# Optimization experiments

Measured on AMD Instinct MI355X. Metric: run time of the kernel, lower is better.

## Reference

```python
import jax, jax.numpy as jnp
import numpy as np

N_NODES = 50000
N_EDGES = 800000
IN, HID, OUT = 128, 128, 64


def gcn_layer(x, W, b, src, dst, n):
    """PyG GCNConv: add self-loops, symmetric normalization, linear, scatter-add, bias."""
    loop = jnp.arange(n, dtype=src.dtype)
    s = jnp.concatenate([src, loop])  # message sources
    d = jnp.concatenate([dst, loop])  # message destinations
    deg = jax.ops.segment_sum(jnp.ones(s.shape[0], dtype=x.dtype), d, num_segments=n)
    dinv = jnp.where(deg > 0, jax.lax.rsqrt(deg), jnp.zeros_like(deg))
    norm = dinv[s] * dinv[d]  # [E+N]
    h = x @ W                 # dense transform first (PyG order)
    agg = jax.ops.segment_sum(h[s] * norm[:, None], d, num_segments=n)  # [N, out]
    return agg + b


def setup_inputs() -> dict:
    key = jax.random.key(0)
    ks = jax.random.split(key, 8)
    x = jax.random.normal(ks[0], (N_NODES, IN), dtype=jnp.float32)
    edge_index = jax.random.randint(ks[1], (2, N_EDGES), 0, N_NODES, dtype=jnp.int32)
    s = 0.05
    W1 = jax.random.normal(ks[2], (IN, HID), dtype=jnp.float32) * s
    b1 = jnp.zeros((HID,), dtype=jnp.float32)
    W2 = jax.random.normal(ks[3], (HID, HID), dtype=jnp.float32) * s
    b2 = jnp.zeros((HID,), dtype=jnp.float32)
    W3 = jax.random.normal(ks[4], (HID, OUT), dtype=jnp.float32) * s
    b3 = jnp.zeros((OUT,), dtype=jnp.float32)
    return {"x": x, "edge_index": edge_index, "W1": W1, "b1": b1,
            "W2": W2, "b2": b2, "W3": W3, "b3": b3}


def reference(x, edge_index, W1, b1, W2, b2, W3, b3):
    src, dst = edge_index[0], edge_index[1]
    n = x.shape[0]
    # dropout is identity in eval mode; ReLU follows every layer (incl. last) as in source
    h = jax.nn.relu(gcn_layer(x, W1, b1, src, dst, n))
    h = jax.nn.relu(gcn_layer(h, W2, b2, src, dst, n))
    h = jax.nn.relu(gcn_layer(h, W3, b3, src, dst, n))
    return jax.nn.log_softmax(h, axis=1)
```

## Files before the change

### kernel.cpp

```cpp
#include <hip/hip_runtime.h>
#include <math.h>


typedef __attribute__((ext_vector_type(8))) short short8;
typedef __attribute__((ext_vector_type(4))) float f32x4;

#define PADROW 50115
#define CAP 64
#define NPART 8

__device__ inline unsigned short f2bf(float x) {
    unsigned int u = __float_as_uint(x);
    u += 0x7fffu + ((u >> 16) & 1u);
    return (unsigned short)(u >> 16);
}
__device__ inline float blo(unsigned int v) { return __uint_as_float(v << 16); }
__device__ inline float bhi(unsigned int v) { return __uint_as_float(v & 0xffff0000u); }


__global__ void prep0_kernel(int* __restrict__ deg, int N,
                             unsigned int* __restrict__ col32, int colw,
                             const float* __restrict__ W1, unsigned short* __restrict__ W1t,
                             const float* __restrict__ W2, unsigned short* __restrict__ W2t,
                             const float* __restrict__ W3, unsigned short* __restrict__ W3t,
                             unsigned short* __restrict__ hbuf) {
    int i = blockIdx.x * blockDim.x + threadIdx.x;
    if (i < N) deg[i] = 0;
    if (i < colw) col32[i] = 0xC3C3C3C3u;
    if (i < 16384) {
        int k = i >> 7, n = i & 127;
        W1t[(size_t)n * 128 + k] = f2bf(W1[i]);
    } else if (i < 32768) {
        int j = i - 16384;
        int k = j >> 7, n = j & 127;
        W2t[(size_t)n * 128 + k] = f2bf(W2[j]);
    } else if (i < 40960) {
        int j = i - 32768;
        int k = j >> 6, n = j & 63;
        W3t[(size_t)n * 128 + k] = f2bf(W3[j]);
    }
    if (i < 16)
        ((uint4*)(hbuf + (size_t)PADROW * 128))[i] = make_uint4(0, 0, 0, 0);
}

__global__ void hist_rank_kernel(const int* __restrict__ dst, int* __restrict__ deg,
                                 unsigned short* __restrict__ rank, int E) {
    int e = blockIdx.x * blockDim.x + threadIdx.x;
    if (e < E) rank[e] = (unsigned short)atomicAdd(&deg[dst[e]], 1);
}

__global__ void scatter_ell_kernel(const int* __restrict__ src, const int* __restrict__ dst,
                                   const unsigned short* __restrict__ rank,
                                   unsigned short* __restrict__ col_ell,
                                   int E, int N, int nblk_per_part) {
    int part = blockIdx.x & (NPART - 1);
    int blk  = blockIdx.x / NPART;
    int npr = (N + NPART - 1) / NPART;
    int lo = part * npr;
    int hi = min(N, lo + npr);
    int stride = nblk_per_part * blockDim.x;
    for (int e = blk * blockDim.x + threadIdx.x; e < E; e += stride) {
        int d = dst[e];
        if (d >= lo && d < hi) {
            int rk = (int)rank[e];
            if (rk < CAP) col_ell[(size_t)d * CAP + rk] = (unsigned short)src[e];
        }
    }
}

template<int H, bool AF32>
__global__ __launch_bounds__(256) void gemm_mfma(const void* __restrict__ Av,
                                                 const unsigned short* __restrict__ Wt,
                                                 const int* __restrict__ deg,
                                                 unsigned short* __restrict__ C, int M) {
    __shared__ __attribute__((aligned(16))) unsigned short As[128][136];
    __shared__ __attribute__((aligned(16))) unsigned short Ws[H][136];
    int tid = threadIdx.x;
    int row0 = blockIdx.x * 128;
    if (AF32) {
        const float* A = (const float*)Av;
        #pragma unroll
        for (int g = tid; g < 128 * 32; g += 256) {
            int r = g >> 5, c = g & 31;
            int gr = row0 + r;
            ushort4 o = make_ushort4(0, 0, 0, 0);
            if (gr < M) {
                float4 v = *(const float4*)(A + (size_t)gr * 128 + c * 4);
                o.x = f2bf(v.x); o.y = f2bf(v.y); o.z = f2bf(v.z); o.w = f2bf(v.w);
            }
            *(ushort4*)&As[r][c * 4] = o;
        }
    } else {
        const unsigned short* A = (const unsigned short*)Av;
        #pragma unroll
        for (int g = tid; g < 128 * 16; g += 256) {
            int r = g >> 4, c = g & 15;
            int gr = row0 + r;
            uint4 v = make_uint4(0, 0, 0, 0);
            if (gr < M) v = *(const uint4*)(A + (size_t)gr * 128 + c * 8);
            *(uint4*)&As[r][c * 8] = v;
        }
    }
    #pragma unroll
    for (int g = tid; g < H * 16; g += 256) {
        int r = g >> 4, c = g & 15;
        *(uint4*)&Ws[r][c * 8] = *(const uint4*)(Wt + (size_t)r * 128 + c * 8);
    }
    if (H == 64 && blockIdx.x == 0 && tid < 8)
        ((uint4*)(C + (size_t)PADROW * 64))[tid] = make_uint4(0, 0, 0, 0);
    __syncthreads();

    int wave = tid >> 6, lane = tid & 63;
    int lr = lane & 15;
    int lk = (lane >> 4) * 8;

    short8 af[2][4];
    float dv[2][4];
    #pragma unroll
    for (int t = 0; t < 2; ++t) {
        int base = wave * 32 + t * 16;
        #pragma unroll
        for (int ks = 0; ks < 4; ++ks)
            af[t][ks] = *(const short8*)&As[base + lr][ks * 32 + lk];
        #pragma unroll
        for (int r = 0; r < 4; ++r) {
            int grow = row0 + base + (lane >> 4) * 4 + r;
            dv[t][r] = (grow < M) ? rsqrtf((float)deg[grow] + 1.0f) : 0.0f;
        }
    }

    #pragma unroll
    for (int ct = 0; ct < H / 16; ++ct) {
        f32x4 acc0 = {0.f, 0.f, 0.f, 0.f};
        f32x4 acc1 = {0.f, 0.f, 0.f, 0.f};
        #pragma unroll
        for (int ks = 0; ks < 4; ++ks) {
            short8 wf = *(const short8*)&Ws[ct * 16 + lr][ks * 32 + lk];
            acc0 = __builtin_amdgcn_mfma_f32_16x16x32_bf16(af[0][ks], wf, acc0, 0, 0, 0);
            acc1 = __builtin_amdgcn_mfma_f32_16x16x32_bf16(af[1][ks], wf, acc1, 0, 0, 0);
        }
        int gcol = ct * 16 + lr;
        #pragma unroll
        for (int r = 0; r < 4; ++r) {
            int g0 = row0 + wave * 32 + (lane >> 4) * 4 + r;
            if (g0 < M) C[(size_t)g0 * H + gcol] = f2bf(acc0[r] * dv[0][r]);
            int g1 = g0 + 16;
            if (g1 < M) C[(size_t)g1 * H + gcol] = f2bf(acc1[r] * dv[1][r]);
        }
    }
}

__global__ __launch_bounds__(256) void spmm128_kernel(const uint2* __restrict__ h2,
                                                      const unsigned short* __restrict__ col_ell,
                                                      const int* __restrict__ deg,
                                                      const float* __restrict__ bias,
                                                      uint2* __restrict__ out2, int N) {
    int wid = blockIdx.x * 4 + (threadIdx.x >> 6);
    int lane = threadIdx.x & 63;
    if (wid >= N) return;
    int half = lane >> 5;
    int c    = lane & 31;
    size_t base = (size_t)wid * CAP;
    int dg = deg[wid];
    float a0 = 0.f, a1 = 0.f, a2 = 0.f, a3 = 0.f;
    if (half == 0) {
        uint2 hv = h2[(size_t)wid * 32 + c];
        a0 = blo(hv.x); a1 = bhi(hv.x); a2 = blo(hv.y); a3 = bhi(hv.y);
    }
    {
        int s[12]; uint2 g[12];
        #pragma unroll
        for (int u = 0; u < 12; ++u) s[u] = (int)col_ell[base + 2 * u + half];
        #pragma unroll
        for (int u = 0; u < 12; ++u) g[u] = h2[(size_t)s[u] * 32 + c];
        #pragma unroll
        for (int u = 0; u < 12; ++u) {
            a0 += blo(g[u].x); a1 += bhi(g[u].x);
            a2 += blo(g[u].y); a3 += bhi(g[u].y);
        }
    }
    if (dg > 24) {
        int s[12]; uint2 g[12];
        #pragma unroll
        for (int u = 0; u < 12; ++u) s[u] = (int)col_ell[base + 24 + 2 * u + half];
        #pragma unroll
        for (int u = 0; u < 12; ++u) g[u] = h2[(size_t)s[u] * 32 + c];
        #pragma unroll
        for (int u = 0; u < 12; ++u) {
            a0 += blo(g[u].x); a1 += bhi(g[u].x);
            a2 += blo(g[u].y); a3 += bhi(g[u].y);
        }
        if (dg > 48) {
            int s[8]; uint2 g[8];
            #pragma unroll
            for (int u = 0; u < 8; ++u) s[u] = (int)col_ell[base + 48 + 2 * u + half];
            #pragma unroll
            for (int u = 0; u < 8; ++u) g[u] = h2[(size_t)s[u] * 32 + c];
            #pragma unroll
            for (int u = 0; u < 8; ++u) {
                a0 += blo(g[u].x); a1 += bhi(g[u].x);
                a2 += blo(g[u].y); a3 += bhi(g[u].y);
            }
        }
    }
    a0 += __shfl_xor(a0, 32);
    a1 += __shfl_xor(a1, 32);
    a2 += __shfl_xor(a2, 32);
    a3 += __shfl_xor(a3, 32);
    float dv = rsqrtf((float)dg + 1.0f);
    float4 b4 = ((const float4*)bias)[c];
    a0 = fmaxf(fmaf(a0, dv, b4.x), 0.0f);
    a1 = fmaxf(fmaf(a1, dv, b4.y), 0.0f);
    a2 = fmaxf(fmaf(a2, dv, b4.z), 0.0f);
    a3 = fmaxf(fmaf(a3, dv, b4.w), 0.0f);
    if (half == 0) {
        uint2 o;
        o.x = (unsigned int)f2bf(a0) | ((unsigned int)f2bf(a1) << 16);
        o.y = (unsigned int)f2bf(a2) | ((unsigned int)f2bf(a3) << 16);
        out2[(size_t)wid * 32 + c] = o;
    }
}

__global__ __launch_bounds__(256) void spmm64_lsm_kernel(const unsigned int* __restrict__ h1,
                                                         const unsigned short* __restrict__ col_ell,
                                                         const int* __restrict__ deg,
                                                         const float* __restrict__ bias,
                                                         float2* __restrict__ out2, int N) {
    int wid = blockIdx.x * 4 + (threadIdx.x >> 6);
    int lane = threadIdx.x & 63;
    if (wid >= N) return;
    int half = lane >> 5;
    int c    = lane & 31;
    size_t base = (size_t)wid * CAP;
    int dg = deg[wid];
    float a0 = 0.f, a1 = 0.f;
    if (half == 0) {
        unsigned int hv = h1[(size_t)wid * 32 + c];
        a0 = blo(hv); a1 = bhi(hv);
    }
    {
        int s[12]; unsigned int g[12];
        #pragma unroll
        for (int u = 0; u < 12; ++u) s[u] = (int)col_ell[base + 2 * u + half];
        #pragma unroll
        for (int u = 0; u < 12; ++u) g[u] = h1[(size_t)s[u] * 32 + c];
        #pragma unroll
        for (int u = 0; u < 12; ++u) { a0 += blo(g[u]); a1 += bhi(g[u]); }
    }
    if (dg > 24) {
        int s[12]; unsigned int g[12];
        #pragma unroll
        for (int u = 0; u < 12; ++u) s[u] = (int)col_ell[base + 24 + 2 * u + half];
        #pragma unroll
        for (int u = 0; u < 12; ++u) g[u] = h1[(size_t)s[u] * 32 + c];
        #pragma unroll
        for (int u = 0; u < 12; ++u) { a0 += blo(g[u]); a1 += bhi(g[u]); }
        if (dg > 48) {
            int s[8]; unsigned int g[8];
            #pragma unroll
            for (int u = 0; u < 8; ++u) s[u] = (int)col_ell[base + 48 + 2 * u + half];
            #pragma unroll
            for (int u = 0; u < 8; ++u) g[u] = h1[(size_t)s[u] * 32 + c];
            #pragma unroll
            for (int u = 0; u < 8; ++u) { a0 += blo(g[u]); a1 += bhi(g[u]); }
        }
    }
    a0 += __shfl_xor(a0, 32);
    a1 += __shfl_xor(a1, 32);
    float dv = rsqrtf((float)dg + 1.0f);
    float2 b2 = ((const float2*)bias)[c];
    a0 = fmaxf(fmaf(a0, dv, b2.x), 0.0f);
    a1 = fmaxf(fmaf(a1, dv, b2.y), 0.0f);
    float m = fmaxf(a0, a1);
    #pragma unroll
    for (int off = 16; off; off >>= 1) m = fmaxf(m, __shfl_xor(m, off));
    float ssum = expf(a0 - m) + expf(a1 - m);
    #pragma unroll
    for (int off = 16; off; off >>= 1) ssum += __shfl_xor(ssum, off);
    float lse = m + logf(ssum);
    if (half == 0) {
        float2 o;
        o.x = a0 - lse;
        o.y = a1 - lse;
        out2[(size_t)wid * 32 + c] = o;
    }
}


extern "C" void kernel_launch(void* const* d_in, const int* in_sizes, int n_in,
                              void* d_out, int out_size, void* d_ws, size_t ws_size,
                              hipStream_t stream) {
    const float* x  = (const float*)d_in[0];
    const int*   ei = (const int*)d_in[1];
    const float* W1 = (const float*)d_in[2];
    const float* b1 = (const float*)d_in[3];
    const float* W2 = (const float*)d_in[4];
    const float* b2 = (const float*)d_in[5];
    const float* W3 = (const float*)d_in[6];
    const float* b3 = (const float*)d_in[7];
    float* out = (float*)d_out;

    const int IN = 128, HID = 128, OUT = 64;
    int N = in_sizes[0] / IN;
    int E = in_sizes[1] / 2;
    const int* srcp = ei;
    const int* dstp = ei + E;

    char* p = (char*)d_ws;
    auto alloc = [&](size_t bytes) {
        char* r = p;
        p += (bytes + 255) & ~(size_t)255;
        return r;
    };
    int* deg = (int*)alloc((size_t)N * 4);
    unsigned short* rank16  = (unsigned short*)alloc((size_t)E * 2);
    unsigned short* col_ell = (unsigned short*)alloc((size_t)N * CAP * 2);
    unsigned short* W1t  = (unsigned short*)alloc((size_t)IN * HID * 2);
    unsigned short* W2t  = (unsigned short*)alloc((size_t)HID * HID * 2);
    unsigned short* W3t  = (unsigned short*)alloc((size_t)HID * OUT * 2);
    unsigned short* hbuf = (unsigned short*)alloc((size_t)(PADROW + 1) * HID * 2);
    unsigned short* abuf = (unsigned short*)alloc((size_t)N * HID * 2);

    int colw = N * CAP / 2;
    int prep0_grid = (max(colw, 40960) + 255) / 256;
    prep0_kernel<<<prep0_grid, 256, 0, stream>>>(deg, N, (unsigned int*)col_ell, colw,
                                                 W1, W1t, W2, W2t, W3, W3t, hbuf);
    hist_rank_kernel<<<(E + 255) / 256, 256, 0, stream>>>(dstp, deg, rank16, E);
    int nblk_per_part = 512;
    scatter_ell_kernel<<<NPART * nblk_per_part, 256, 0, stream>>>(srcp, dstp, rank16,
                                                                  col_ell, E, N, nblk_per_part);

    int nwave_blocks = (N + 3) / 4;
    int gemm_blocks = (N + 127) / 128;

    gemm_mfma<128, true><<<gemm_blocks, 256, 0, stream>>>(x, W1t, deg, hbuf, N);
    spmm128_kernel<<<nwave_blocks, 256, 0, stream>>>((const uint2*)hbuf, col_ell, deg,
                                                     b1, (uint2*)abuf, N);
    gemm_mfma<128, false><<<gemm_blocks, 256, 0, stream>>>(abuf, W2t, deg, hbuf, N);
    spmm128_kernel<<<nwave_blocks, 256, 0, stream>>>((const uint2*)hbuf, col_ell, deg,
                                                     b2, (uint2*)abuf, N);
    gemm_mfma<64, false><<<gemm_blocks, 256, 0, stream>>>(abuf, W3t, deg, hbuf, N);
    spmm64_lsm_kernel<<<nwave_blocks, 256, 0, stream>>>((const unsigned int*)hbuf, col_ell, deg,
                                                        b3, (float2*)out, N);
}
```

Measured before the change: 181.8 us.

## Fuse ELL histogram into scatter and remap spmm64 to one node per half-wave

Merges the histogram/rank kernel into the partitioned ELL scatter kernel, so each edge takes its slot with an atomicAdd on deg directly. This drops one launch and the rank buffer's write and read. It also changes the final spmm64+log_softmax kernel so that each 32-lane half-wave handles one node, instead of a full wave split into two halves. Each half-wave now gathers all neighbors itself, which removes the cross-half shuffle. The cost is more registers from the 24-wide unroll and longer serial gather chains per node.

```diff
diff --git a/kernel.cpp b/kernel.cpp
--- a/kernel.cpp
+++ b/kernel.cpp
@@ -43,16 +43,9 @@
         ((uint4*)(hbuf + (size_t)PADROW * 128))[i] = make_uint4(0, 0, 0, 0);
 }
 
-__global__ void hist_rank_kernel(const int* __restrict__ dst, int* __restrict__ deg,
-                                 unsigned short* __restrict__ rank, int E) {
-    int e = blockIdx.x * blockDim.x + threadIdx.x;
-    if (e < E) rank[e] = (unsigned short)atomicAdd(&deg[dst[e]], 1);
-}
-
-__global__ void scatter_ell_kernel(const int* __restrict__ src, const int* __restrict__ dst,
-                                   const unsigned short* __restrict__ rank,
-                                   unsigned short* __restrict__ col_ell,
-                                   int E, int N, int nblk_per_part) {
+__global__ void build_ell_kernel(const int* __restrict__ src, const int* __restrict__ dst,
+                                 int* __restrict__ deg, unsigned short* __restrict__ col_ell,
+                                 int E, int N, int nblk_per_part) {
     int part = blockIdx.x & (NPART - 1);
     int blk  = blockIdx.x / NPART;
     int npr = (N + NPART - 1) / NPART;
@@ -62,7 +55,7 @@
     for (int e = blk * blockDim.x + threadIdx.x; e < E; e += stride) {
         int d = dst[e];
         if (d >= lo && d < hi) {
-            int rk = (int)rank[e];
+            int rk = atomicAdd(&deg[d], 1);
             if (rk < CAP) col_ell[(size_t)d * CAP + rk] = (unsigned short)src[e];
         }
     }
@@ -221,52 +214,45 @@
     }
 }
 
-__global__ __launch_bounds__(256) void spmm64_lsm_kernel(const unsigned int* __restrict__ h1,
-                                                         const unsigned short* __restrict__ col_ell,
-                                                         const int* __restrict__ deg,
-                                                         const float* __restrict__ bias,
-                                                         float2* __restrict__ out2, int N) {
-    int wid = blockIdx.x * 4 + (threadIdx.x >> 6);
-    int lane = threadIdx.x & 63;
+__global__ __launch_bounds__(256, 4) void spmm64_lsm_kernel(const unsigned int* __restrict__ h1,
+                                                            const unsigned short* __restrict__ col_ell,
+                                                            const int* __restrict__ deg,
+                                                            const float* __restrict__ bias,
+                                                            float2* __restrict__ out2, int N) {
+    int wid = blockIdx.x * 8 + (threadIdx.x >> 5);
+    int c = threadIdx.x & 31;
     if (wid >= N) return;
-    int half = lane >> 5;
-    int c    = lane & 31;
     size_t base = (size_t)wid * CAP;
     int dg = deg[wid];
-    float a0 = 0.f, a1 = 0.f;
-    if (half == 0) {
-        unsigned int hv = h1[(size_t)wid * 32 + c];
-        a0 = blo(hv); a1 = bhi(hv);
-    }
+    unsigned int hv = h1[(size_t)wid * 32 + c];
+    float a0 = blo(hv), a1 = bhi(hv);
     {
-        int s[12]; unsigned int g[12];
-        #pragma unroll
-        for (int u = 0; u < 12; ++u) s[u] = (int)col_ell[base + 2 * u + half];
-        #pragma unroll
-        for (int u = 0; u < 12; ++u) g[u] = h1[(size_t)s[u] * 32 + c];
-        #pragma unroll
-        for (int u = 0; u < 12; ++u) { a0 += blo(g[u]); a1 += bhi(g[u]); }
+        int s[24]; unsigned int g[24];
+        #pragma unroll
+        for (int u = 0; u < 24; ++u) s[u] = (int)col_ell[base + u];
+        #pragma unroll
+        for (int u = 0; u < 24; ++u) g[u] = h1[(size_t)s[u] * 32 + c];
+        #pragma unroll
+        for (int u = 0; u < 24; ++u) { a0 += blo(g[u]); a1 += bhi(g[u]); }
     }
     if (dg > 24) {
-        int s[12]; unsigned int g[12];
-        #pragma unroll
-        for (int u = 0; u < 12; ++u) s[u] = (int)col_ell[base + 24 + 2 * u + half];
-        #pragma unroll
-        for (int u = 0; u < 12; ++u) g[u] = h1[(size_t)s[u] * 32 + c];
-        #pragma unroll
-        for (int u = 0; u < 12; ++u) { a0 += blo(g[u]); a1 += bhi(g[u]); }
+        int s[24]; unsigned int g[24];
+        #pragma unroll
+        for (int u = 0; u < 24; ++u) s[u] = (int)col_ell[base + 24 + u];
+        #pragma unroll
+        for (int u = 0; u < 24; ++u) g[u] = h1[(size_t)s[u] * 32 + c];
+        #pragma unroll
+        for (int u = 0; u < 24; ++u) { a0 += blo(g[u]); a1 += bhi(g[u]); }
         if (dg > 48) {
-            int s[8]; unsigned int g[8];
-            #pragma unroll
-            for (int u = 0; u < 8; ++u) s[u] = (int)col_ell[base + 48 + 2 * u + half];
-            #pragma unroll
-            for (int u = 0; u < 8; ++u) g[u] = h1[(size_t)s[u] * 32 + c];
-            #pragma unroll
-            for (int u = 0; u < 8; ++u) { a0 += blo(g[u]); a1 += bhi(g[u]); }
-        }
-    }
-    a0 += __shfl_xor(a0, 32);
-    a1 += __shfl_xor(a1, 32);
+            int s[16]; unsigned int g[16];
+            #pragma unroll
+            for (int u = 0; u < 16; ++u) s[u] = (int)col_ell[base + 48 + u];
+            #pragma unroll
+            for (int u = 0; u < 16; ++u) g[u] = h1[(size_t)s[u] * 32 + c];
+            #pragma unroll
+            for (int u = 0; u < 16; ++u) { a0 += blo(g[u]); a1 += bhi(g[u]); }
+        }
+    }
     float dv = rsqrtf((float)dg + 1.0f);
     float2 b2 = ((const float2*)bias)[c];
     a0 = fmaxf(fmaf(a0, dv, b2.x), 0.0f);
@@ -278,12 +264,10 @@
     #pragma unroll
     for (int off = 16; off; off >>= 1) ssum += __shfl_xor(ssum, off);
     float lse = m + logf(ssum);
-    if (half == 0) {
-        float2 o;
-        o.x = a0 - lse;
-        o.y = a1 - lse;
-        out2[(size_t)wid * 32 + c] = o;
-    }
+    float2 o;
+    o.x = a0 - lse;
+    o.y = a1 - lse;
+    out2[(size_t)wid * 32 + c] = o;
 }
 
 
@@ -313,7 +297,6 @@
         return r;
     };
     int* deg = (int*)alloc((size_t)N * 4);
-    unsigned short* rank16  = (unsigned short*)alloc((size_t)E * 2);
     unsigned short* col_ell = (unsigned short*)alloc((size_t)N * CAP * 2);
     unsigned short* W1t  = (unsigned short*)alloc((size_t)IN * HID * 2);
     unsigned short* W2t  = (unsigned short*)alloc((size_t)HID * HID * 2);
@@ -325,21 +308,21 @@
     int prep0_grid = (max(colw, 40960) + 255) / 256;
     prep0_kernel<<<prep0_grid, 256, 0, stream>>>(deg, N, (unsigned int*)col_ell, colw,
                                                  W1, W1t, W2, W2t, W3, W3t, hbuf);
-    hist_rank_kernel<<<(E + 255) / 256, 256, 0, stream>>>(dstp, deg, rank16, E);
     int nblk_per_part = 512;
-    scatter_ell_kernel<<<NPART * nblk_per_part, 256, 0, stream>>>(srcp, dstp, rank16,
-                                                                  col_ell, E, N, nblk_per_part);
-
-    int nwave_blocks = (N + 3) / 4;
+    build_ell_kernel<<<NPART * nblk_per_part, 256, 0, stream>>>(srcp, dstp, deg, col_ell,
+                                                                E, N, nblk_per_part);
+
+    int spmm128_blocks = (N + 3) / 4;
+    int spmm64_blocks = (N + 7) / 8;
     int gemm_blocks = (N + 127) / 128;
 
     gemm_mfma<128, true><<<gemm_blocks, 256, 0, stream>>>(x, W1t, deg, hbuf, N);
-    spmm128_kernel<<<nwave_blocks, 256, 0, stream>>>((const uint2*)hbuf, col_ell, deg,
-                                                     b1, (uint2*)abuf, N);
+    spmm128_kernel<<<spmm128_blocks, 256, 0, stream>>>((const uint2*)hbuf, col_ell, deg,
+                                                       b1, (uint2*)abuf, N);
     gemm_mfma<128, false><<<gemm_blocks, 256, 0, stream>>>(abuf, W2t, deg, hbuf, N);
-    spmm128_kernel<<<nwave_blocks, 256, 0, stream>>>((const uint2*)hbuf, col_ell, deg,
-                                                     b2, (uint2*)abuf, N);
+    spmm128_kernel<<<spmm128_blocks, 256, 0, stream>>>((const uint2*)hbuf, col_ell, deg,
+                                                       b2, (uint2*)abuf, N);
     gemm_mfma<64, false><<<gemm_blocks, 256, 0, stream>>>(abuf, W3t, deg, hbuf, N);
-    spmm64_lsm_kernel<<<nwave_blocks, 256, 0, stream>>>((const unsigned int*)hbuf, col_ell, deg,
-                                                        b3, (float2*)out, N);
-}
+    spmm64_lsm_kernel<<<spmm64_blocks, 256, 0, stream>>>((const unsigned int*)hbuf, col_ell, deg,
+                                                         b3, (float2*)out, N);
+}
```

After: 163.6 us. -10.0%, faster.
